# Performance work log

Measured on AMD Instinct MI355X. Metric: run time of the kernel, lower is better.

Reference implementation:

```python
import jax, jax.numpy as jnp
import numpy as np

N = 100000      # nodes
E = 3200000     # edges
F_IN = 64       # num_input_features
HID = 3         # hardcoded hidden width in GCN
F_OUT = 256     # gcn_output_features
F_TR = 512      # transformer_feature_size


def setup_inputs() -> dict:
    key = jax.random.key(0)
    ks = jax.random.split(key, 12)
    x = jax.random.normal(ks[0], (N, F_IN), dtype=jnp.float32)
    edge_index = jax.random.randint(ks[1], (2, E), 0, N, dtype=jnp.int64)
    s = 0.05
    # ChebConv1 (K=2): two weight mats [in,out] + bias
    W0a = jax.random.normal(ks[2], (F_IN, HID), jnp.float32) * s
    W1a = jax.random.normal(ks[3], (F_IN, HID), jnp.float32) * s
    b1 = jax.random.normal(ks[4], (HID,), jnp.float32) * s
    # ChebConv2 (K=2)
    W0b = jax.random.normal(ks[5], (HID, F_OUT), jnp.float32) * s
    W1b = jax.random.normal(ks[6], (HID, F_OUT), jnp.float32) * s
    b2 = jax.random.normal(ks[7], (F_OUT,), jnp.float32) * s
    # final Linear
    Wl = jax.random.normal(ks[8], (F_OUT, F_TR), jnp.float32) * s
    bl = jax.random.normal(ks[9], (F_TR,), jnp.float32) * s
    return {"x": x, "edge_index": edge_index, "W0a": W0a, "W1a": W1a,
            "b1": b1, "W0b": W0b, "W1b": W1b, "b2": b2, "Wl": Wl, "bl": bl}


def _cheb_norm(edge_index, num_nodes):
    # PyG ChebConv.__norm__ with sym normalization, lambda_max=2.0:
    # L_hat = 2L/2 - I = -D^{-1/2} A D^{-1/2} (diagonal cancels to 0).
    src, dst = edge_index[0], edge_index[1]
    w = jnp.where(src != dst, 1.0, 0.0).astype(jnp.float32)  # remove_self_loops
    deg = jnp.zeros((num_nodes,), jnp.float32).at[src].add(w)
    dinv = jnp.where(deg > 0, jax.lax.rsqrt(jnp.maximum(deg, 1.0)), 0.0)
    return -dinv[src] * w * dinv[dst]  # [E]


def _cheb_conv(x, edge_index, norm, W0, W1, b):
    # K=2 Chebyshev: Tx0 = x, Tx1 = L_hat @ x (scatter-add over edges)
    src, dst = edge_index[0], edge_index[1]
    Tx1 = jnp.zeros_like(x).at[dst].add(norm[:, None] * x[src])
    return x @ W0 + Tx1 @ W1 + b


def reference(x, edge_index, W0a, W1a, b1, W0b, W1b, b2, Wl, bl):
    norm = _cheb_norm(edge_index, x.shape[0])
    h = jax.nn.relu(_cheb_conv(x, edge_index, norm, W0a, W1a, b1))
    h = jax.nn.relu(_cheb_conv(h, edge_index, norm, W0b, W1b, b2))
    return h @ Wl + bl
```

## Files before the change

kernel.cpp:

```cpp
#include <hip/hip_runtime.h>
#include <hip/hip_bf16.h>


#define MAXNB 1024
#define BSH 7
#define BSZ 128
#define SRC_BITS 20
#define SRC_MASK ((1u << SRC_BITS) - 1u)
#define EPB 16384

typedef __attribute__((ext_vector_type(8))) short short8;
typedef __attribute__((ext_vector_type(4))) float f32x4;

static __device__ inline unsigned short f2bf(float f) {
    union { float f; unsigned u; } v; v.f = f;
    unsigned r = (v.u + 0x7fffu + ((v.u >> 16) & 1u)) >> 16;
    return (unsigned short)r;
}

__global__ __launch_bounds__(256) void k_prep(const float* __restrict__ Wl,
                                              unsigned short* __restrict__ WlT,
                                              unsigned* __restrict__ subcurD,
                                              unsigned* __restrict__ subcurS) {
    __shared__ float tile[32][33];
    int t = threadIdx.x, tx = t & 31, ty = t >> 5;
    if (blockIdx.x == 0) {
        for (int i = t; i < MAXNB; i += 256) { subcurD[i] = 0u; subcurS[i] = 0u; }
    }
    int kb = (blockIdx.x & 7) * 32;
    int cb = (blockIdx.x >> 3) * 32;
#pragma unroll
    for (int r = 0; r < 4; r++) {
        int k = kb + ty + r * 8;
        tile[ty + r * 8][tx] = Wl[(size_t)k * 512 + cb + tx];
    }
    __syncthreads();
#pragma unroll
    for (int r = 0; r < 4; r++) {
        int c = cb + ty + r * 8;
        WlT[(size_t)c * 256 + kb + tx] = f2bf(tile[tx][ty + r * 8]);
    }
}

__global__ __launch_bounds__(1024) void k_hist(const int* __restrict__ ei, int E, int NB,
                                               unsigned* __restrict__ subcurD,
                                               unsigned* __restrict__ subcurS,
                                               unsigned* __restrict__ baseD,
                                               unsigned* __restrict__ baseS) {
    __shared__ unsigned hD[MAXNB], hS[MAXNB];
    int t = threadIdx.x, blk = blockIdx.x;
    for (int i = t; i < NB; i += 1024) { hD[i] = 0u; hS[i] = 0u; }
    __syncthreads();
    int e0 = blk * EPB, e1 = min(e0 + EPB, E);
    if ((E & 3) == 0) {
        int nv = (e1 - e0) >> 2;
        const int4* s4 = (const int4*)(ei + e0);
        const int4* d4 = (const int4*)(ei + (size_t)E + e0);
        for (int i = t; i < nv; i += 1024) {
            int4 ss = s4[i], dd = d4[i];
            if (ss.x != dd.x) { atomicAdd(&hD[dd.x >> BSH], 1u); atomicAdd(&hS[ss.x >> BSH], 1u); }
            if (ss.y != dd.y) { atomicAdd(&hD[dd.y >> BSH], 1u); atomicAdd(&hS[ss.y >> BSH], 1u); }
            if (ss.z != dd.z) { atomicAdd(&hD[dd.z >> BSH], 1u); atomicAdd(&hS[ss.z >> BSH], 1u); }
            if (ss.w != dd.w) { atomicAdd(&hD[dd.w >> BSH], 1u); atomicAdd(&hS[ss.w >> BSH], 1u); }
        }
        for (int e = e0 + (nv << 2) + t; e < e1; e += 1024) {
            int s = ei[e], d = ei[(size_t)E + e];
            if (s != d) { atomicAdd(&hD[d >> BSH], 1u); atomicAdd(&hS[s >> BSH], 1u); }
        }
    } else {
        for (int e = e0 + t; e < e1; e += 1024) {
            int s = ei[e], d = ei[(size_t)E + e];
            if (s != d) { atomicAdd(&hD[d >> BSH], 1u); atomicAdd(&hS[s >> BSH], 1u); }
        }
    }
    __syncthreads();
    unsigned* bD = baseD + (size_t)blk * NB;
    unsigned* bS = baseS + (size_t)blk * NB;
    for (int i = t; i < NB; i += 1024) {
        unsigned h = hD[i];
        if (h) bD[i] = atomicAdd(&subcurD[i], h);
        h = hS[i];
        if (h) bS[i] = atomicAdd(&subcurS[i], h);
    }
}

__global__ __launch_bounds__(1024) void k_scan(const unsigned* __restrict__ totD,
                                               const unsigned* __restrict__ totS,
                                               unsigned* __restrict__ startD,
                                               unsigned* __restrict__ startS, int NB) {
    __shared__ unsigned a[MAXNB], b[MAXNB];
    int t = threadIdx.x;
    for (int i = t; i < NB; i += 1024) a[i] = totD[i];
    __syncthreads();
    unsigned* s = a; unsigned* d = b;
    for (int off = 1; off < NB; off <<= 1) {
        for (int i = t; i < NB; i += 1024)
            d[i] = s[i] + (i >= off ? s[i - off] : 0u);
        __syncthreads();
        unsigned* tmp = s; s = d; d = tmp;
    }
    for (int i = t; i < NB; i += 1024)
        startD[i] = (i == 0) ? 0u : s[i - 1];
    if (t == 0) startD[NB] = s[NB - 1];
    __syncthreads();
    for (int i = t; i < NB; i += 1024) a[i] = totS[i];
    __syncthreads();
    s = a; d = b;
    for (int off = 1; off < NB; off <<= 1) {
        for (int i = t; i < NB; i += 1024)
            d[i] = s[i] + (i >= off ? s[i - off] : 0u);
        __syncthreads();
        unsigned* tmp = s; s = d; d = tmp;
    }
    for (int i = t; i < NB; i += 1024)
        startS[i] = (i == 0) ? 0u : s[i - 1];
    if (t == 0) startS[NB] = s[NB - 1];
}

__global__ __launch_bounds__(1024) void k_place(const int* __restrict__ ei, int E, int NB,
                                                const unsigned* __restrict__ startD,
                                                const unsigned* __restrict__ startS,
                                                const unsigned* __restrict__ baseD,
                                                const unsigned* __restrict__ baseS,
                                                unsigned* __restrict__ dstbin,
                                                unsigned char* __restrict__ srcbin) {
    __shared__ unsigned oD[MAXNB], oS[MAXNB], cD[MAXNB], cS[MAXNB];
    int t = threadIdx.x, blk = blockIdx.x;
    const unsigned* bD = baseD + (size_t)blk * NB;
    const unsigned* bS = baseS + (size_t)blk * NB;
    for (int i = t; i < NB; i += 1024) {
        oD[i] = startD[i] + bD[i];
        oS[i] = startS[i] + bS[i];
        cD[i] = 0u; cS[i] = 0u;
    }
    __syncthreads();
    int e0 = blk * EPB, e1 = min(e0 + EPB, E);
    if ((E & 3) == 0) {
        int nv = (e1 - e0) >> 2;
        const int4* s4 = (const int4*)(ei + e0);
        const int4* d4 = (const int4*)(ei + (size_t)E + e0);
        for (int i = t; i < nv; i += 1024) {
            int4 ss = s4[i], dd = d4[i];
            int sa[4] = {ss.x, ss.y, ss.z, ss.w};
            int da[4] = {dd.x, dd.y, dd.z, dd.w};
#pragma unroll
            for (int j = 0; j < 4; j++) {
                int s = sa[j], d = da[j];
                if (s != d) {
                    int bk = d >> BSH;
                    unsigned pos = oD[bk] + atomicAdd(&cD[bk], 1u);
                    dstbin[pos] = ((unsigned)(d & (BSZ - 1)) << SRC_BITS) | (unsigned)s;
                    int bs = s >> BSH;
                    unsigned ps = oS[bs] + atomicAdd(&cS[bs], 1u);
                    srcbin[ps] = (unsigned char)(s & (BSZ - 1));
                }
            }
        }
        for (int e = e0 + (nv << 2) + t; e < e1; e += 1024) {
            int s = ei[e], d = ei[(size_t)E + e];
            if (s != d) {
                int bk = d >> BSH;
                unsigned pos = oD[bk] + atomicAdd(&cD[bk], 1u);
                dstbin[pos] = ((unsigned)(d & (BSZ - 1)) << SRC_BITS) | (unsigned)s;
                int bs = s >> BSH;
                unsigned ps = oS[bs] + atomicAdd(&cS[bs], 1u);
                srcbin[ps] = (unsigned char)(s & (BSZ - 1));
            }
        }
    } else {
        for (int e = e0 + t; e < e1; e += 1024) {
            int s = ei[e], d = ei[(size_t)E + e];
            if (s != d) {
                int bk = d >> BSH;
                unsigned pos = oD[bk] + atomicAdd(&cD[bk], 1u);
                dstbin[pos] = ((unsigned)(d & (BSZ - 1)) << SRC_BITS) | (unsigned)s;
                int bs = s >> BSH;
                unsigned ps = oS[bs] + atomicAdd(&cS[bs], 1u);
                srcbin[ps] = (unsigned char)(s & (BSZ - 1));
            }
        }
    }
}

__global__ __launch_bounds__(256) void k_sortdeg(
    const unsigned* __restrict__ dstbin, const unsigned* __restrict__ startD,
    unsigned* __restrict__ dsorted, unsigned* __restrict__ nodeoff,
    const unsigned char* __restrict__ srcbin, const unsigned* __restrict__ startS,
    const float* __restrict__ x, const float* __restrict__ W0a,
    const float* __restrict__ W1a, float* __restrict__ dinv,
    float4* __restrict__ a3v, float4* __restrict__ y3v, int N) {
    __shared__ unsigned cnt[BSZ], tmp[BSZ], cur[BSZ];
    __shared__ unsigned cnt4[4][BSZ];
    __shared__ float w0[192], w1[192];
    __shared__ float dl[BSZ];
    int t = threadIdx.x, b = blockIdx.x;
    if (t < 192) { w0[t] = W0a[t]; w1[t] = W1a[t]; }
    if (t < BSZ) cnt[t] = 0u;
    for (int i = t; i < 4 * BSZ; i += 256) ((unsigned*)cnt4)[i] = 0u;
    __syncthreads();
    unsigned d0 = startD[b], d1 = startD[b + 1];
    for (unsigned e = d0 + t; e < d1; e += 256)
        atomicAdd(&cnt[dstbin[e] >> SRC_BITS], 1u);
    unsigned s0 = startS[b], s1 = startS[b + 1];
    int rep = t & 3;
    for (unsigned i = s0 + t; i < s1; i += 256) atomicAdd(&cnt4[rep][srcbin[i]], 1u);
    __syncthreads();
    for (int off = 1; off < BSZ; off <<= 1) {
        if (t < BSZ) tmp[t] = cnt[t] + (t >= off ? cnt[t - off] : 0u);
        __syncthreads();
        if (t < BSZ) cnt[t] = tmp[t];
        __syncthreads();
    }
    if (t <= BSZ) {
        unsigned ex = (t == 0) ? 0u : cnt[t - 1];
        int idx = b * BSZ + t;
        if (idx <= N) nodeoff[idx] = d0 + ex;
        if (t < BSZ) cur[t] = ex;
    }
    __syncthreads();
    for (unsigned e = d0 + t; e < d1; e += 256) {
        unsigned p = dstbin[e];
        unsigned pos = d0 + atomicAdd(&cur[p >> SRC_BITS], 1u);
        dsorted[pos] = p & SRC_MASK;
    }
    if (t < BSZ) {
        unsigned c = cnt4[0][t] + cnt4[1][t] + cnt4[2][t] + cnt4[3][t];
        float dv = c ? rsqrtf((float)c) : 0.f;
        dl[t] = dv;
        int g = b * BSZ + t;
        if (g < N) dinv[g] = dv;
    }
    __syncthreads();
    int q = t & 3;
#pragma unroll
    for (int pass = 0; pass < 2; pass++) {
        int nn = (t >> 2) + pass * 64;
        int node = b * BSZ + nn;
        float acc[6] = {0.f, 0.f, 0.f, 0.f, 0.f, 0.f};
        if (node < N) {
            const float4* xr = (const float4*)(x + (size_t)node * 64 + q * 16);
#pragma unroll
            for (int i = 0; i < 4; i++) {
                float4 v = xr[i];
                float xs[4] = {v.x, v.y, v.z, v.w};
#pragma unroll
                for (int c = 0; c < 4; c++) {
                    int f = q * 16 + i * 4 + c;
                    float xi = xs[c];
                    acc[0] += xi * w0[f * 3 + 0];
                    acc[1] += xi * w0[f * 3 + 1];
                    acc[2] += xi * w0[f * 3 + 2];
                    acc[3] += xi * w1[f * 3 + 0];
                    acc[4] += xi * w1[f * 3 + 1];
                    acc[5] += xi * w1[f * 3 + 2];
                }
            }
        }
#pragma unroll
        for (int m = 1; m < 4; m <<= 1)
#pragma unroll
            for (int j = 0; j < 6; j++) acc[j] += __shfl_xor(acc[j], m, 64);
        if (q == 0 && node < N) {
            a3v[node] = make_float4(acc[0], acc[1], acc[2], 0.f);
            y3v[node] = make_float4(acc[3], acc[4], acc[5], dl[nn]);
        }
    }
}

__global__ __launch_bounds__(512) void k_tgather(
    const unsigned* __restrict__ dsorted, const unsigned* __restrict__ nodeoff,
    const float4* __restrict__ v4, const float* __restrict__ dinv,
    const float4* __restrict__ a3v, const float* __restrict__ b1,
    float4* __restrict__ outv, int N, int phase) {
    int t = threadIdx.x;
    int g = t >> 3, q = t & 7;
    int node = blockIdx.x * 64 + g;
    if (node >= N) return;
    float dv = dinv[node];
    unsigned o0 = nodeoff[node], o1 = nodeoff[node + 1];
    float s0 = 0.f, s1 = 0.f, s2 = 0.f;
#pragma unroll 2
    for (unsigned e = o0 + q; e < o1; e += 8) {
        float4 v = v4[dsorted[e]];
        float nm = -v.w * dv;
        s0 += nm * v.x; s1 += nm * v.y; s2 += nm * v.z;
    }
#pragma unroll
    for (int m = 1; m < 8; m <<= 1) {
        s0 += __shfl_xor(s0, m, 64);
        s1 += __shfl_xor(s1, m, 64);
        s2 += __shfl_xor(s2, m, 64);
    }
    if (q == 0) {
        if (phase == 1) {
            float4 a = a3v[node];
            outv[node] = make_float4(fmaxf(s0 + a.x + b1[0], 0.f),
                                     fmaxf(s1 + a.y + b1[1], 0.f),
                                     fmaxf(s2 + a.z + b1[2], 0.f), dv);
        } else {
            outv[node] = make_float4(s0, s1, s2, 0.f);
        }
    }
}

__global__ __launch_bounds__(256) void k_final_mfma(
    const float4* __restrict__ h1v, const float4* __restrict__ t2r,
    const float* __restrict__ W0b, const float* __restrict__ W1b,
    const float* __restrict__ b2, const unsigned short* __restrict__ WlT,
    const float* __restrict__ bl, float* __restrict__ out, int N) {
    __shared__ unsigned short h2s[64 * 256];
    __shared__ float4 u4[64][2];
    char* h2b = (char*)h2s;
    int t = threadIdx.x, b = blockIdx.x;
    int n0 = b * 64;

    if (t < 64) {
        int g = n0 + t;
        u4[t][0] = (g < N) ? h1v[g] : make_float4(0.f, 0.f, 0.f, 0.f);
    } else if (t < 128) {
        int g = n0 + t - 64;
        u4[t - 64][1] = (g < N) ? t2r[g] : make_float4(0.f, 0.f, 0.f, 0.f);
    }
    __syncthreads();

    {
        int k0 = (t & 127) * 2;
        int rh = (t >> 7) * 32;
        float w00a = W0b[k0],       w00b = W0b[k0 + 1];
        float w01a = W0b[256 + k0], w01b = W0b[256 + k0 + 1];
        float w02a = W0b[512 + k0], w02b = W0b[512 + k0 + 1];
        float w10a = W1b[k0],       w10b = W1b[k0 + 1];
        float w11a = W1b[256 + k0], w11b = W1b[256 + k0 + 1];
        float w12a = W1b[512 + k0], w12b = W1b[512 + k0 + 1];
        float bka = b2[k0], bkb = b2[k0 + 1];
        int kbyte = k0 * 2;
#pragma unroll
        for (int r = 0; r < 32; r++) {
            int rr = rh + r;
            float4 h = u4[rr][0];
            float4 v = u4[rr][1];
            float za = bka + h.x * w00a + h.y * w01a + h.z * w02a
                           + v.x * w10a + v.y * w11a + v.z * w12a;
            float zb = bkb + h.x * w00b + h.y * w01b + h.z * w02b
                           + v.x * w10b + v.y * w11b + v.z * w12b;
            za = fmaxf(za, 0.f); zb = fmaxf(zb, 0.f);
            unsigned pk = ((unsigned)f2bf(zb) << 16) | (unsigned)f2bf(za);
            int byte = rr * 512 + (kbyte ^ ((rr & 7) << 4));
            *(unsigned*)(h2b + byte) = pk;
        }
    }
    __syncthreads();

    int w = t >> 6, l = t & 63;
    int cb0 = (int)blockIdx.y * 128 + w * 32;
    int lrow = l & 15, lkb = (l >> 4) * 8, cq = (l >> 4) * 4;

    f32x4 acc[4][2];
#pragma unroll
    for (int rt = 0; rt < 4; rt++)
#pragma unroll
        for (int ct = 0; ct < 2; ct++) acc[rt][ct] = (f32x4)0.f;

#pragma unroll
    for (int ks = 0; ks < 8; ks++) {
        int kel = ks * 32 + lkb;
        short8 af[4];
#pragma unroll
        for (int rt = 0; rt < 4; rt++) {
            int r = rt * 16 + lrow;
            int byte = r * 512 + ((kel * 2) ^ ((r & 7) << 4));
            af[rt] = *(const short8*)(h2b + byte);
        }
        short8 bf[2];
#pragma unroll
        for (int ct = 0; ct < 2; ct++) {
            int c = cb0 + ct * 16 + lrow;
            bf[ct] = *(const short8*)(WlT + (size_t)c * 256 + kel);
        }
#pragma unroll
        for (int rt = 0; rt < 4; rt++)
#pragma unroll
            for (int ct = 0; ct < 2; ct++)
                acc[rt][ct] = __builtin_amdgcn_mfma_f32_16x16x32_bf16(
                    bf[ct], af[rt], acc[rt][ct], 0, 0, 0);
    }

    f32x4 blv[2];
#pragma unroll
    for (int ct = 0; ct < 2; ct++)
        blv[ct] = *(const f32x4*)(bl + cb0 + ct * 16 + cq);

    float* sp = (float*)h2s;
#pragma unroll
    for (int rb = 0; rb < 2; rb++) {
        __syncthreads();
#pragma unroll
        for (int rr = 0; rr < 2; rr++) {
            int rt = rb * 2 + rr;
            int row_local = rr * 16 + lrow;
            int swz = (row_local & 7) << 4;
            int colb = w * 32 + cq;
#pragma unroll
            for (int ct = 0; ct < 2; ct++) {
                int byte = row_local * 512 + (((colb + ct * 16) * 4) ^ swz);
                f32x4 sv = acc[rt][ct] + blv[ct];
                *(f32x4*)((char*)sp + byte) = sv;
            }
        }
        __syncthreads();
#pragma unroll
        for (int j = 0; j < 4; j++) {
            int f = j * 256 + t;
            int row_local = f >> 5;
            int col4 = f & 31;
            int swz = (row_local & 7) << 4;
            int byte = row_local * 512 + ((col4 * 16) ^ swz);
            f32x4 sv = *(const f32x4*)((const char*)sp + byte);
            int row = n0 + rb * 32 + row_local;
            if (row < N) {
                __builtin_nontemporal_store(
                    sv, (f32x4*)(out + (size_t)row * 512 +
                                 (size_t)blockIdx.y * 128 + col4 * 4));
            }
        }
    }
}

extern "C" void kernel_launch(void* const* d_in, const int* in_sizes, int n_in,
                              void* d_out, int out_size, void* d_ws, size_t ws_size,
                              hipStream_t stream) {
    const float* x   = (const float*)d_in[0];
    const int*   ei  = (const int*)d_in[1];
    const float* W0a = (const float*)d_in[2];
    const float* W1a = (const float*)d_in[3];
    const float* b1  = (const float*)d_in[4];
    const float* W0b = (const float*)d_in[5];
    const float* W1b = (const float*)d_in[6];
    const float* b2  = (const float*)d_in[7];
    const float* Wl  = (const float*)d_in[8];
    const float* bl  = (const float*)d_in[9];
    float* out = (float*)d_out;

    const int N = in_sizes[0] / 64;
    const int E = in_sizes[1] / 2;
    const int NB = (N + BSZ - 1) >> BSH;
    const int CB = (E + EPB - 1) / EPB;
    const int NB64 = (N + 63) / 64;

    char* base = (char*)d_ws;
    size_t off = 0;
    auto alloc = [&](size_t bytes) {
        void* p = base + off;
        off = (off + bytes + 255) & ~(size_t)255;
        return p;
    };
    unsigned* subcurD = (unsigned*)alloc(MAXNB * 4);
    unsigned* subcurS = (unsigned*)alloc(MAXNB * 4);
    unsigned* startD  = (unsigned*)alloc((MAXNB + 1) * 4);
    unsigned* startS  = (unsigned*)alloc((MAXNB + 1) * 4);
    unsigned* baseD   = (unsigned*)alloc((size_t)CB * NB * 4);
    unsigned* baseS   = (unsigned*)alloc((size_t)CB * NB * 4);
    unsigned* dstbin  = (unsigned*)alloc((size_t)E * 4);
    unsigned* dsorted = (unsigned*)alloc((size_t)E * 4);
    unsigned* nodeoff = (unsigned*)alloc((size_t)(N + 1) * 4);
    unsigned char* srcbin = (unsigned char*)alloc((size_t)E);
    float* dinv = (float*)alloc((size_t)N * 4);
    float* a3v  = (float*)alloc((size_t)N * 16);
    float* y3v  = (float*)alloc((size_t)N * 16);
    float* h1v  = (float*)alloc((size_t)N * 16);
    float* t2r  = (float*)alloc((size_t)N * 16);
    unsigned short* WlT = (unsigned short*)alloc(512 * 256 * 2);

    k_prep<<<128, 256, 0, stream>>>(Wl, WlT, subcurD, subcurS);
    k_hist<<<CB, 1024, 0, stream>>>(ei, E, NB, subcurD, subcurS, baseD, baseS);
    k_scan<<<1, 1024, 0, stream>>>(subcurD, subcurS, startD, startS, NB);
    k_place<<<CB, 1024, 0, stream>>>(ei, E, NB, startD, startS, baseD, baseS,
                                     dstbin, srcbin);
    k_sortdeg<<<NB, 256, 0, stream>>>(dstbin, startD, dsorted, nodeoff,
                                      srcbin, startS, x, W0a, W1a, dinv,
                                      (float4*)a3v, (float4*)y3v, N);
    k_tgather<<<NB64, 512, 0, stream>>>(dsorted, nodeoff, (const float4*)y3v, dinv,
                                        (const float4*)a3v, b1, (float4*)h1v, N, 1);
    k_tgather<<<NB64, 512, 0, stream>>>(dsorted, nodeoff, (const float4*)h1v, dinv,
                                        (const float4*)a3v, b1, (float4*)t2r, N, 2);
    k_final_mfma<<<dim3(NB64, 4), 256, 0, stream>>>(
        (const float4*)h1v, (const float4*)t2r, W0b, W1b, b2, WlT, bl, out, N);
}
```

Measured before the change: 212.0 us.

## Fuse weight prep, histogram and scan into one kernel via last-block scan

```diff
diff --git a/kernel.cpp b/kernel.cpp
--- a/kernel.cpp
+++ b/kernel.cpp
@@ -18,37 +18,42 @@
     return (unsigned short)r;
 }
 
-__global__ __launch_bounds__(256) void k_prep(const float* __restrict__ Wl,
-                                              unsigned short* __restrict__ WlT,
-                                              unsigned* __restrict__ subcurD,
-                                              unsigned* __restrict__ subcurS) {
+__global__ __launch_bounds__(1024) void k_histprep(
+    const int* __restrict__ ei, int E, int NB, int CB,
+    unsigned* __restrict__ subcurD, unsigned* __restrict__ subcurS,
+    unsigned* __restrict__ donecnt,
+    unsigned* __restrict__ baseD, unsigned* __restrict__ baseS,
+    unsigned* __restrict__ startD, unsigned* __restrict__ startS,
+    const float* __restrict__ Wl, unsigned short* __restrict__ WlT) {
+    __shared__ unsigned hD[MAXNB], hS[MAXNB];
     __shared__ float tile[32][33];
-    int t = threadIdx.x, tx = t & 31, ty = t >> 5;
-    if (blockIdx.x == 0) {
-        for (int i = t; i < MAXNB; i += 256) { subcurD[i] = 0u; subcurS[i] = 0u; }
-    }
-    int kb = (blockIdx.x & 7) * 32;
-    int cb = (blockIdx.x >> 3) * 32;
-#pragma unroll
-    for (int r = 0; r < 4; r++) {
-        int k = kb + ty + r * 8;
-        tile[ty + r * 8][tx] = Wl[(size_t)k * 512 + cb + tx];
-    }
-    __syncthreads();
-#pragma unroll
-    for (int r = 0; r < 4; r++) {
-        int c = cb + ty + r * 8;
-        WlT[(size_t)c * 256 + kb + tx] = f2bf(tile[tx][ty + r * 8]);
-    }
-}
-
-__global__ __launch_bounds__(1024) void k_hist(const int* __restrict__ ei, int E, int NB,
-                                               unsigned* __restrict__ subcurD,
-                                               unsigned* __restrict__ subcurS,
-                                               unsigned* __restrict__ baseD,
-                                               unsigned* __restrict__ baseS) {
-    __shared__ unsigned hD[MAXNB], hS[MAXNB];
+    __shared__ unsigned lastFlag;
     int t = threadIdx.x, blk = blockIdx.x;
+
+    if (blk >= CB) {
+        int id = blk - CB;
+        bool act = t < 256;
+        int tx = t & 31, ty = (t & 255) >> 5;
+        int kb = (id & 7) * 32;
+        int cb = (id >> 3) * 32;
+        if (act) {
+#pragma unroll
+            for (int r = 0; r < 4; r++) {
+                int k = kb + ty + r * 8;
+                tile[ty + r * 8][tx] = Wl[(size_t)k * 512 + cb + tx];
+            }
+        }
+        __syncthreads();
+        if (act) {
+#pragma unroll
+            for (int r = 0; r < 4; r++) {
+                int c = cb + ty + r * 8;
+                WlT[(size_t)c * 256 + kb + tx] = f2bf(tile[tx][ty + r * 8]);
+            }
+        }
+        return;
+    }
+
     for (int i = t; i < NB; i += 1024) { hD[i] = 0u; hS[i] = 0u; }
     __syncthreads();
     int e0 = blk * EPB, e1 = min(e0 + EPB, E);
@@ -82,39 +87,45 @@
         h = hS[i];
         if (h) bS[i] = atomicAdd(&subcurS[i], h);
     }
-}
-
-__global__ __launch_bounds__(1024) void k_scan(const unsigned* __restrict__ totD,
-                                               const unsigned* __restrict__ totS,
-                                               unsigned* __restrict__ startD,
-                                               unsigned* __restrict__ startS, int NB) {
-    __shared__ unsigned a[MAXNB], b[MAXNB];
-    int t = threadIdx.x;
-    for (int i = t; i < NB; i += 1024) a[i] = totD[i];
-    __syncthreads();
-    unsigned* s = a; unsigned* d = b;
-    for (int off = 1; off < NB; off <<= 1) {
+
+    __threadfence();
+    if (t == 0) {
+        unsigned prev = atomicAdd(donecnt, 1u);
+        lastFlag = (prev == (unsigned)(CB - 1)) ? 1u : 0u;
+    }
+    __syncthreads();
+    if (!lastFlag) return;
+    __threadfence();
+
+    for (int i = t; i < NB; i += 1024) hD[i] = atomicAdd(&subcurD[i], 0u);
+    __syncthreads();
+    {
+        unsigned* s = hD; unsigned* d = hS;
+        for (int off = 1; off < NB; off <<= 1) {
+            for (int i = t; i < NB; i += 1024)
+                d[i] = s[i] + (i >= off ? s[i - off] : 0u);
+            __syncthreads();
+            unsigned* tmp = s; s = d; d = tmp;
+        }
         for (int i = t; i < NB; i += 1024)
-            d[i] = s[i] + (i >= off ? s[i - off] : 0u);
-        __syncthreads();
-        unsigned* tmp = s; s = d; d = tmp;
-    }
-    for (int i = t; i < NB; i += 1024)
-        startD[i] = (i == 0) ? 0u : s[i - 1];
-    if (t == 0) startD[NB] = s[NB - 1];
-    __syncthreads();
-    for (int i = t; i < NB; i += 1024) a[i] = totS[i];
-    __syncthreads();
-    s = a; d = b;
-    for (int off = 1; off < NB; off <<= 1) {
+            startD[i] = (i == 0) ? 0u : s[i - 1];
+        if (t == 0) startD[NB] = s[NB - 1];
+    }
+    __syncthreads();
+    for (int i = t; i < NB; i += 1024) hD[i] = atomicAdd(&subcurS[i], 0u);
+    __syncthreads();
+    {
+        unsigned* s = hD; unsigned* d = hS;
+        for (int off = 1; off < NB; off <<= 1) {
+            for (int i = t; i < NB; i += 1024)
+                d[i] = s[i] + (i >= off ? s[i - off] : 0u);
+            __syncthreads();
+            unsigned* tmp = s; s = d; d = tmp;
+        }
         for (int i = t; i < NB; i += 1024)
-            d[i] = s[i] + (i >= off ? s[i - off] : 0u);
-        __syncthreads();
-        unsigned* tmp = s; s = d; d = tmp;
-    }
-    for (int i = t; i < NB; i += 1024)
-        startS[i] = (i == 0) ? 0u : s[i - 1];
-    if (t == 0) startS[NB] = s[NB - 1];
+            startS[i] = (i == 0) ? 0u : s[i - 1];
+        if (t == 0) startS[NB] = s[NB - 1];
+    }
 }
 
 __global__ __launch_bounds__(1024) void k_place(const int* __restrict__ ei, int E, int NB,
@@ -456,6 +467,7 @@
     };
     unsigned* subcurD = (unsigned*)alloc(MAXNB * 4);
     unsigned* subcurS = (unsigned*)alloc(MAXNB * 4);
+    unsigned* donecnt = (unsigned*)alloc(256);
     unsigned* startD  = (unsigned*)alloc((MAXNB + 1) * 4);
     unsigned* startS  = (unsigned*)alloc((MAXNB + 1) * 4);
     unsigned* baseD   = (unsigned*)alloc((size_t)CB * NB * 4);
@@ -471,9 +483,11 @@
     float* t2r  = (float*)alloc((size_t)N * 16);
     unsigned short* WlT = (unsigned short*)alloc(512 * 256 * 2);
 
-    k_prep<<<128, 256, 0, stream>>>(Wl, WlT, subcurD, subcurS);
-    k_hist<<<CB, 1024, 0, stream>>>(ei, E, NB, subcurD, subcurS, baseD, baseS);
-    k_scan<<<1, 1024, 0, stream>>>(subcurD, subcurS, startD, startS, NB);
+    hipMemsetAsync(subcurD, 0, 2 * MAXNB * 4 + 256, stream);
+
+    k_histprep<<<CB + 128, 1024, 0, stream>>>(ei, E, NB, CB, subcurD, subcurS,
+                                              donecnt, baseD, baseS, startD,
+                                              startS, Wl, WlT);
     k_place<<<CB, 1024, 0, stream>>>(ei, E, NB, startD, startS, baseD, baseS,
                                      dstbin, srcbin);
     k_sortdeg<<<NB, 256, 0, stream>>>(dstbin, startD, dsorted, nodeoff,
```

Measured after the change: 268.5 us. +26.6%, slower.
